# Optimization experiments

Measured on AMD Instinct MI355X. Metric: run time of the kernel, lower is better.

Reference implementation:

```python
import jax, jax.numpy as jnp
import numpy as np

B, T, H = 8, 2048, 1024
P = 64           # num_attention_project
N = 4096         # config.n (bias table length), N >= 2T-1
WINDOW = 64      # relative_attention
NEG = -10000.0


def setup_inputs() -> dict:
    key = jax.random.key(0)
    ks = jax.random.split(key, 10)
    s = 1.0 / np.sqrt(H)
    sp = 1.0 / np.sqrt(P)
    sb = 1.0 / np.sqrt(N)
    return {
        "attn_input": jax.random.normal(ks[0], (B, T, H), dtype=jnp.float32),
        "attention_mask": jnp.ones((B, T), dtype=jnp.float32),
        # Linear weights stored as [in, out] so y = x @ W + b
        "Wq": jax.random.uniform(ks[1], (H, P), minval=-s, maxval=s),
        "bq": jnp.zeros((P,), jnp.float32),
        "Wk": jax.random.uniform(ks[2], (H, P), minval=-s, maxval=s),
        "bk": jnp.zeros((P,), jnp.float32),
        "Wv": jax.random.uniform(ks[3], (H, P), minval=-s, maxval=s),
        "bv": jnp.zeros((P,), jnp.float32),
        "Wo": jax.random.uniform(ks[4], (P, H), minval=-sp, maxval=sp),
        "bo": jnp.zeros((H,), jnp.float32),
        "bias": jax.random.uniform(ks[5], (N,), minval=-sb, maxval=sb),
    }


def reference(attn_input, attention_mask, Wq, bq, Wk, bk, Wv, bv, Wo, bo, bias):
    q = attn_input @ Wq + bq            # [B,T,P]
    k = attn_input @ Wk + bk
    v = attn_input @ Wv + bv
    scores = jnp.einsum("btp,bsp->bts", q, k) / jnp.sqrt(jnp.float32(P))  # [B,T,T]
    # padding mask: note original broadcasts over COLUMNS via unsqueeze(-1)
    scores = scores + (1.0 - attention_mask)[:, :, None] * NEG
    # circulant window mask: keep |i-j| <= WINDOW (all ones if WINDOW >= T)
    i = jnp.arange(T)
    rel = i[:, None] - i[None, :]       # i - j
    win = (jnp.abs(rel) <= WINDOW) | (WINDOW >= T)
    scores = scores + jnp.where(win, 0.0, NEG)[None, :, :]
    # gathered learnable relative-position bias: bias[n//2 - i + j]
    scores = scores + bias[N // 2 - rel][None, :, :]
    attn = jax.nn.softmax(scores, axis=-1)
    out = jnp.einsum("bts,bsp->btp", attn, v)
    return out @ Wo + bo                # [B,T,H]
```

## Files before the change

### kernel.cpp

```cpp
#include <hip/hip_runtime.h>

using bf16x8 = __attribute__((ext_vector_type(8))) short;
using f32x4  = __attribute__((ext_vector_type(4))) float;

static __device__ inline unsigned short f2bf(float f) {
  unsigned int u = __float_as_uint(f);
  u += 0x7fffu + ((u >> 16) & 1u);
  return (unsigned short)(u >> 16);
}
static __device__ inline unsigned int pk2(float a, float b) {
  return (unsigned int)f2bf(a) | ((unsigned int)f2bf(b) << 16);
}

#define ROW16_MAX(x) { \
  { int _t = __builtin_amdgcn_update_dpp(0, __float_as_int(x), 0x121, 0xf, 0xf, true); x = fmaxf(x, __int_as_float(_t)); } \
  { int _t = __builtin_amdgcn_update_dpp(0, __float_as_int(x), 0x122, 0xf, 0xf, true); x = fmaxf(x, __int_as_float(_t)); } \
  { int _t = __builtin_amdgcn_update_dpp(0, __float_as_int(x), 0x124, 0xf, 0xf, true); x = fmaxf(x, __int_as_float(_t)); } \
  { int _t = __builtin_amdgcn_update_dpp(0, __float_as_int(x), 0x128, 0xf, 0xf, true); x = fmaxf(x, __int_as_float(_t)); } }
#define ROW16_SUM(x) { \
  { int _t = __builtin_amdgcn_update_dpp(0, __float_as_int(x), 0x121, 0xf, 0xf, true); x += __int_as_float(_t); } \
  { int _t = __builtin_amdgcn_update_dpp(0, __float_as_int(x), 0x122, 0xf, 0xf, true); x += __int_as_float(_t); } \
  { int _t = __builtin_amdgcn_update_dpp(0, __float_as_int(x), 0x124, 0xf, 0xf, true); x += __int_as_float(_t); } \
  { int _t = __builtin_amdgcn_update_dpp(0, __float_as_int(x), 0x128, 0xf, 0xf, true); x += __int_as_float(_t); } }

__global__ __launch_bounds__(256) void prep_kernel(
    const float* __restrict__ Wq, const float* __restrict__ Wk, const float* __restrict__ Wv,
    const float* __restrict__ Wo, const float* __restrict__ bq, const float* __restrict__ bk,
    const float* __restrict__ bv,
    unsigned short* __restrict__ Wt, unsigned short* __restrict__ Wot, float* __restrict__ bqkv)
{
  int idx = blockIdx.x * 256 + threadIdx.x;
  if (idx < 192 * 1024) {
    int n = idx >> 10, k = idx & 1023;
    const float* W = (n < 64) ? Wq : (n < 128) ? Wk : Wv;
    Wt[idx] = f2bf(W[k * 64 + (n & 63)]);
  } else if (idx < 192 * 1024 + 1024 * 64) {
    int j = idx - 192 * 1024;
    int n = j >> 6, k = j & 63;
    Wot[j] = f2bf(Wo[k * 1024 + n]);
  } else if (idx < 192 * 1024 + 1024 * 64 + 192) {
    int n = idx - (192 * 1024 + 1024 * 64);
    bqkv[n] = (n < 64) ? bq[n] : (n < 128) ? bk[n - 64] : bv[n - 128];
  }
}

__global__ __launch_bounds__(256) void qkv_gemm(
    const float* __restrict__ X, const unsigned short* __restrict__ Wt,
    const float* __restrict__ bqkv, unsigned short* __restrict__ qkvb)
{
  __shared__ __align__(16) unsigned short As[2][32 * 72];
  __shared__ __align__(16) unsigned short Bs[2][96 * 72];
  int t = threadIdx.x;
  int lane = t & 63, w = t >> 6;
  int m0 = (blockIdx.x >> 1) * 32;
  int nbase = (blockIdx.x & 1) * 96;
  int mg = w & 1, ng = w >> 1;
  int col = lane & 15, quad = lane >> 4;
  f32x4 acc[3] = {};

  int rowA = t >> 3, cA = t & 7;
  const float* srcA = X + (size_t)(m0 + rowA) * 1024 + cA * 8;
  const unsigned short* srcB = Wt + (size_t)(nbase + rowA) * 1024 + cA * 8;

  float4 f0 = *(const float4*)(srcA);
  float4 f1 = *(const float4*)(srcA + 4);
  uint4 b0 = *(const uint4*)(srcB);
  uint4 b1 = *(const uint4*)(srcB + 32 * 1024);
  uint4 b2 = *(const uint4*)(srcB + 64 * 1024);

  for (int ks = 0; ks < 16; ++ks) {
    int cur = ks & 1;
    {
      uint4 p;
      p.x = pk2(f0.x, f0.y); p.y = pk2(f0.z, f0.w);
      p.z = pk2(f1.x, f1.y); p.w = pk2(f1.z, f1.w);
      *(uint4*)(As[cur] + rowA * 72 + cA * 8) = p;
      *(uint4*)(Bs[cur] + rowA * 72 + cA * 8) = b0;
      *(uint4*)(Bs[cur] + (rowA + 32) * 72 + cA * 8) = b1;
      *(uint4*)(Bs[cur] + (rowA + 64) * 72 + cA * 8) = b2;
    }
    if (ks < 15) {
      const float* sA = srcA + (ks + 1) * 64;
      f0 = *(const float4*)(sA);
      f1 = *(const float4*)(sA + 4);
      const unsigned short* sB = srcB + (ks + 1) * 64;
      b0 = *(const uint4*)(sB);
      b1 = *(const uint4*)(sB + 32 * 1024);
      b2 = *(const uint4*)(sB + 64 * 1024);
    }
    __syncthreads();
    #pragma unroll
    for (int kk = 0; kk < 64; kk += 32) {
      int ko = kk + quad * 8;
      bf16x8 a = *(const bf16x8*)(As[cur] + (mg * 16 + col) * 72 + ko);
      #pragma unroll
      for (int ns = 0; ns < 3; ++ns) {
        bf16x8 b = *(const bf16x8*)(Bs[cur] + ((ng * 3 + ns) * 16 + col) * 72 + ko);
        acc[ns] = __builtin_amdgcn_mfma_f32_16x16x32_bf16(a, b, acc[ns], 0, 0, 0);
      }
    }
  }
  #pragma unroll
  for (int ns = 0; ns < 3; ++ns)
    #pragma unroll
    for (int r = 0; r < 4; ++r) {
      int m = m0 + mg * 16 + quad * 4 + r;
      int n = nbase + ng * 48 + ns * 16 + col;
      qkvb[(size_t)m * 192 + n] = f2bf(acc[ns][r] + bqkv[n]);
    }
}

__global__ __launch_bounds__(256) void band_attn(
    const unsigned short* __restrict__ qkvb, const float* __restrict__ bias,
    unsigned short* __restrict__ attnout)
{
  __shared__ __align__(16) unsigned short Kl[192 * 72];
  __shared__ __align__(16) unsigned short Vt[64 * 216];
  __shared__ __align__(16) unsigned short Ps[4 * 16 * 168];
  __shared__ float biasL[129];

  int t = threadIdx.x;
  int lane = t & 63, w = t >> 6;
  int col = lane & 15, quad = lane >> 4;
  int bidx = blockIdx.x;
  int b = bidx >> 5;
  int i0 = (bidx & 31) * 64;
  int jw = i0 - 64;
  const unsigned short* qbase = qkvb + (size_t)(b << 11) * 192;

  int iq = i0 + w * 16;
  const unsigned short* qr = qbase + (size_t)(iq + col) * 192 + quad * 8;
  bf16x8 aq0 = *(const bf16x8*)(qr);
  bf16x8 aq1 = *(const bf16x8*)(qr + 32);

  if (t < 129) biasL[t] = bias[1984 + t];
  #pragma unroll
  for (int it = 0; it < 12; ++it) {
    int idx = it * 256 + t;
    int row = idx >> 4;
    int c = idx & 15;
    int jb = jw + row;
    int jc = jb < 0 ? 0 : (jb > 2047 ? 2047 : jb);
    const unsigned short* src = qbase + (size_t)jc * 192 + 64 + c * 8;
    uint4 v = *(const uint4*)src;
    if (c < 8) {
      *(uint4*)(Kl + row * 72 + c * 8) = v;
    } else {
      union { uint4 u; unsigned short s[8]; } uv; uv.u = v;
      int p0 = (c - 8) * 8;
      #pragma unroll
      for (int e = 0; e < 8; ++e) Vt[(p0 + e) * 216 + row] = uv.s[e];
    }
  }
  {
    int p = t >> 2, c0 = 192 + (t & 3) * 4;
    *(uint2*)(Vt + p * 216 + c0) = make_uint2(0u, 0u);
  }
  __syncthreads();

  f32x4 s[9];
  #pragma unroll
  for (int t9 = 0; t9 < 9; ++t9) {
    int krow = ((w + t9) * 16 + col) * 72;
    bf16x8 kb0 = *(const bf16x8*)(Kl + krow + quad * 8);
    bf16x8 kb1 = *(const bf16x8*)(Kl + krow + 32 + quad * 8);
    f32x4 z = {};
    z = __builtin_amdgcn_mfma_f32_16x16x32_bf16(aq0, kb0, z, 0, 0, 0);
    s[t9] = __builtin_amdgcn_mfma_f32_16x16x32_bf16(aq1, kb1, z, 0, 0, 0);
  }
  int q4 = quad * 4;
  float mrow[4] = {-3e38f, -3e38f, -3e38f, -3e38f};
  #pragma unroll
  for (int t9 = 0; t9 < 9; ++t9) {
    int j = iq - 64 + t9 * 16 + col;
    #pragma unroll
    for (int r = 0; r < 4; ++r) {
      int diff = q4 + r + 64 - t9 * 16 - col;
      bool valid = (j >= 0) & (j < 2048) & (diff >= -64) & (diff <= 64);
      int bi = 64 - diff; bi = bi < 0 ? 0 : (bi > 128 ? 128 : bi);
      float sv = valid ? (s[t9][r] * 0.125f + biasL[bi]) : -3e38f;
      s[t9][r] = sv;
      mrow[r] = fmaxf(mrow[r], sv);
    }
  }
  #pragma unroll
  for (int r = 0; r < 4; ++r) ROW16_MAX(mrow[r]);
  unsigned short* Pw = Ps + w * (16 * 168);
  float lsum[4] = {0.f, 0.f, 0.f, 0.f};
  #pragma unroll
  for (int t9 = 0; t9 < 9; ++t9)
    #pragma unroll
    for (int r = 0; r < 4; ++r) {
      float p = __expf(s[t9][r] - mrow[r]);
      lsum[r] += p;
      Pw[(q4 + r) * 168 + t9 * 16 + col] = f2bf(p);
    }
  #pragma unroll
  for (int r = 0; r < 4; ++r) {
    ROW16_SUM(lsum[r]);
    Pw[(q4 + r) * 168 + 144 + col] = 0;
  }
  f32x4 o[4] = {};
  #pragma unroll
  for (int kc = 0; kc < 5; ++kc) {
    bf16x8 pa = *(const bf16x8*)(Pw + col * 168 + kc * 32 + quad * 8);
    #pragma unroll
    for (int nt = 0; nt < 4; ++nt) {
      bf16x8 vb = *(const bf16x8*)(Vt + (nt * 16 + col) * 216 + 16 * w + kc * 32 + quad * 8);
      o[nt] = __builtin_amdgcn_mfma_f32_16x16x32_bf16(pa, vb, o[nt], 0, 0, 0);
    }
  }
  float rl[4];
  #pragma unroll
  for (int r = 0; r < 4; ++r) rl[r] = 1.0f / lsum[r];
  #pragma unroll
  for (int nt = 0; nt < 4; ++nt)
    #pragma unroll
    for (int r = 0; r < 4; ++r) {
      int arow = (b << 11) + iq + q4 + r;
      attnout[(size_t)arow * 64 + nt * 16 + col] = f2bf(o[nt][r] * rl[r]);
    }
}

__global__ __launch_bounds__(256) void out_gemm(
    const unsigned short* __restrict__ attn, const unsigned short* __restrict__ Wot,
    const float* __restrict__ bo, float* __restrict__ out)
{
  __shared__ __align__(16) unsigned short As[64 * 72];
  __shared__ __align__(16) unsigned short Bs[128 * 72];
  int t = threadIdx.x, lane = t & 63, w = t >> 6;
  int m0 = (blockIdx.x >> 3) * 64;
  int n0 = (blockIdx.x & 7) * 128;
  #pragma unroll
  for (int r = 0; r < 2; ++r) {
    int tau = t + 256 * r; int row = tau >> 3, c = tau & 7;
    *(uint4*)(As + row * 72 + c * 8) =
        *(const uint4*)(attn + (size_t)(m0 + row) * 64 + c * 8);
  }
  #pragma unroll
  for (int r = 0; r < 4; ++r) {
    int tau = t + 256 * r; int n = tau >> 3, c = tau & 7;
    *(uint4*)(Bs + n * 72 + c * 8) =
        *(const uint4*)(Wot + (size_t)(n0 + n) * 64 + c * 8);
  }
  __syncthreads();
  f32x4 acc[2][4] = {};
  int mg = w & 1, ngg = w >> 1;
  #pragma unroll
  for (int kk = 0; kk < 64; kk += 32) {
    int ko = kk + (lane >> 4) * 8;
    bf16x8 a0 = *(const bf16x8*)(As + (mg * 32 +      (lane & 15)) * 72 + ko);
    bf16x8 a1 = *(const bf16x8*)(As + (mg * 32 + 16 + (lane & 15)) * 72 + ko);
    #pragma unroll
    for (int ns = 0; ns < 4; ++ns) {
      bf16x8 b = *(const bf16x8*)(Bs + ((ngg * 4 + ns) * 16 + (lane & 15)) * 72 + ko);
      acc[0][ns] = __builtin_amdgcn_mfma_f32_16x16x32_bf16(a0, b, acc[0][ns], 0, 0, 0);
      acc[1][ns] = __builtin_amdgcn_mfma_f32_16x16x32_bf16(a1, b, acc[1][ns], 0, 0, 0);
    }
  }
  int col = lane & 15, q = lane >> 4;
  #pragma unroll
  for (int ms = 0; ms < 2; ++ms)
    #pragma unroll
    for (int ns = 0; ns < 4; ++ns)
      #pragma unroll
      for (int r = 0; r < 4; ++r) {
        int mm = m0 + mg * 32 + ms * 16 + q * 4 + r;
        int nn = n0 + (ngg * 4 + ns) * 16 + col;
        out[(size_t)mm * 1024 + nn] = acc[ms][ns][r] + bo[nn];
      }
}

extern "C" void kernel_launch(void* const* d_in, const int* in_sizes, int n_in,
                              void* d_out, int out_size, void* d_ws, size_t ws_size,
                              hipStream_t stream) {
  const float* X    = (const float*)d_in[0];
  const float* Wq   = (const float*)d_in[2];
  const float* bq   = (const float*)d_in[3];
  const float* Wk   = (const float*)d_in[4];
  const float* bk   = (const float*)d_in[5];
  const float* Wv   = (const float*)d_in[6];
  const float* bv   = (const float*)d_in[7];
  const float* Wo   = (const float*)d_in[8];
  const float* bo   = (const float*)d_in[9];
  const float* bias = (const float*)d_in[10];
  float* out = (float*)d_out;
  char* ws = (char*)d_ws;
  unsigned short* qkvb = (unsigned short*)(ws);
  unsigned short* attn = (unsigned short*)(ws + 6291456);
  unsigned short* Wt   = (unsigned short*)(ws + 8388608);
  unsigned short* Wot  = (unsigned short*)(ws + 8781824);
  float*          bqkv = (float*)(ws + 8912896);

  prep_kernel<<<1025, 256, 0, stream>>>(Wq, Wk, Wv, Wo, bq, bk, bv, Wt, Wot, bqkv);
  qkv_gemm<<<1024, 256, 0, stream>>>(X, Wt, bqkv, qkvb);
  band_attn<<<256, 256, 0, stream>>>(qkvb, bias, attn);
  out_gemm<<<2048, 256, 0, stream>>>(attn, Wot, bo, out);
}
```

Before: 167.7 us.

## Split band attention key tiles across wave pairs and unroll QKV GEMM double buffer

The band attention kernel now runs with 512 threads. Each pair of waves splits the 9 key tiles and the 5 PV k-chunks of one 16-row query strip, and the pair combines row max, row sum and partial outputs through shared memory. This raises occupancy and parallelism for a kernel launched with only 256 blocks, at the cost of extra syncs and shared memory. The QKV GEMM loop is also manually unrolled by two with separate register sets for even and odd stages, which removes the dynamic buffer index.

Result: no change. 167.5 us (-0.1%).

```diff
diff --git a/kernel.cpp b/kernel.cpp
--- a/kernel.cpp
+++ b/kernel.cpp
@@ -44,6 +44,34 @@
   }
 }
 
+#define QKV_STORE(BUF, A0, A1, B0, B1, B2) { \
+  uint4 pv_; \
+  pv_.x = pk2(A0.x, A0.y); pv_.y = pk2(A0.z, A0.w); \
+  pv_.z = pk2(A1.x, A1.y); pv_.w = pk2(A1.z, A1.w); \
+  *(uint4*)(As[BUF] + rowA * 72 + cA * 8) = pv_; \
+  *(uint4*)(Bs[BUF] + rowA * 72 + cA * 8) = B0; \
+  *(uint4*)(Bs[BUF] + (rowA + 32) * 72 + cA * 8) = B1; \
+  *(uint4*)(Bs[BUF] + (rowA + 64) * 72 + cA * 8) = B2; }
+
+#define QKV_LOAD(KS, A0, A1, B0, B1, B2) { \
+  const float* sA_ = srcA + (KS) * 64; \
+  A0 = *(const float4*)(sA_); A1 = *(const float4*)(sA_ + 4); \
+  const unsigned short* sB_ = srcB + (KS) * 64; \
+  B0 = *(const uint4*)(sB_); \
+  B1 = *(const uint4*)(sB_ + 32 * 1024); \
+  B2 = *(const uint4*)(sB_ + 64 * 1024); }
+
+#define QKV_MMA(BUF) { \
+  _Pragma("unroll") \
+  for (int kk = 0; kk < 64; kk += 32) { \
+    int ko = kk + quad * 8; \
+    bf16x8 afr = *(const bf16x8*)(As[BUF] + (mg * 16 + col) * 72 + ko); \
+    _Pragma("unroll") \
+    for (int ns = 0; ns < 3; ++ns) { \
+      bf16x8 bfr = *(const bf16x8*)(Bs[BUF] + ((ng * 3 + ns) * 16 + col) * 72 + ko); \
+      acc[ns] = __builtin_amdgcn_mfma_f32_16x16x32_bf16(afr, bfr, acc[ns], 0, 0, 0); \
+    } } }
+
 __global__ __launch_bounds__(256) void qkv_gemm(
     const float* __restrict__ X, const unsigned short* __restrict__ Wt,
     const float* __restrict__ bqkv, unsigned short* __restrict__ qkvb)
@@ -62,43 +90,20 @@
   const float* srcA = X + (size_t)(m0 + rowA) * 1024 + cA * 8;
   const unsigned short* srcB = Wt + (size_t)(nbase + rowA) * 1024 + cA * 8;
 
-  float4 f0 = *(const float4*)(srcA);
-  float4 f1 = *(const float4*)(srcA + 4);
-  uint4 b0 = *(const uint4*)(srcB);
-  uint4 b1 = *(const uint4*)(srcB + 32 * 1024);
-  uint4 b2 = *(const uint4*)(srcB + 64 * 1024);
-
-  for (int ks = 0; ks < 16; ++ks) {
-    int cur = ks & 1;
-    {
-      uint4 p;
-      p.x = pk2(f0.x, f0.y); p.y = pk2(f0.z, f0.w);
-      p.z = pk2(f1.x, f1.y); p.w = pk2(f1.z, f1.w);
-      *(uint4*)(As[cur] + rowA * 72 + cA * 8) = p;
-      *(uint4*)(Bs[cur] + rowA * 72 + cA * 8) = b0;
-      *(uint4*)(Bs[cur] + (rowA + 32) * 72 + cA * 8) = b1;
-      *(uint4*)(Bs[cur] + (rowA + 64) * 72 + cA * 8) = b2;
-    }
-    if (ks < 15) {
-      const float* sA = srcA + (ks + 1) * 64;
-      f0 = *(const float4*)(sA);
-      f1 = *(const float4*)(sA + 4);
-      const unsigned short* sB = srcB + (ks + 1) * 64;
-      b0 = *(const uint4*)(sB);
-      b1 = *(const uint4*)(sB + 32 * 1024);
-      b2 = *(const uint4*)(sB + 64 * 1024);
-    }
+  float4 eA0, eA1; uint4 eB0, eB1, eB2;
+  float4 oA0, oA1; uint4 oB0, oB1, oB2;
+  QKV_LOAD(0, eA0, eA1, eB0, eB1, eB2);
+  QKV_LOAD(1, oA0, oA1, oB0, oB1, oB2);
+
+  for (int ks = 0; ks < 16; ks += 2) {
+    QKV_STORE(0, eA0, eA1, eB0, eB1, eB2);
+    if (ks + 2 < 16) QKV_LOAD(ks + 2, eA0, eA1, eB0, eB1, eB2);
     __syncthreads();
-    #pragma unroll
-    for (int kk = 0; kk < 64; kk += 32) {
-      int ko = kk + quad * 8;
-      bf16x8 a = *(const bf16x8*)(As[cur] + (mg * 16 + col) * 72 + ko);
-      #pragma unroll
-      for (int ns = 0; ns < 3; ++ns) {
-        bf16x8 b = *(const bf16x8*)(Bs[cur] + ((ng * 3 + ns) * 16 + col) * 72 + ko);
-        acc[ns] = __builtin_amdgcn_mfma_f32_16x16x32_bf16(a, b, acc[ns], 0, 0, 0);
-      }
-    }
+    QKV_MMA(0);
+    QKV_STORE(1, oA0, oA1, oB0, oB1, oB2);
+    if (ks + 3 < 16) QKV_LOAD(ks + 3, oA0, oA1, oB0, oB1, oB2);
+    __syncthreads();
+    QKV_MMA(1);
   }
   #pragma unroll
   for (int ns = 0; ns < 3; ++ns)
@@ -110,33 +115,37 @@
     }
 }
 
-__global__ __launch_bounds__(256) void band_attn(
+__global__ __launch_bounds__(512) void band_attn(
     const unsigned short* __restrict__ qkvb, const float* __restrict__ bias,
     unsigned short* __restrict__ attnout)
 {
   __shared__ __align__(16) unsigned short Kl[192 * 72];
   __shared__ __align__(16) unsigned short Vt[64 * 216];
   __shared__ __align__(16) unsigned short Ps[4 * 16 * 168];
+  __shared__ float Osum[4][16][64];
+  __shared__ float Mx[8][16];
+  __shared__ float Lx[8][16];
   __shared__ float biasL[129];
 
   int t = threadIdx.x;
   int lane = t & 63, w = t >> 6;
-  int col = lane & 15, quad = lane >> 4;
+  int p = w >> 1, s = w & 1;
+  int col = lane & 15, quad = lane >> 4, q4 = quad * 4;
   int bidx = blockIdx.x;
   int b = bidx >> 5;
   int i0 = (bidx & 31) * 64;
   int jw = i0 - 64;
   const unsigned short* qbase = qkvb + (size_t)(b << 11) * 192;
 
-  int iq = i0 + w * 16;
+  int iq = i0 + p * 16;
   const unsigned short* qr = qbase + (size_t)(iq + col) * 192 + quad * 8;
   bf16x8 aq0 = *(const bf16x8*)(qr);
   bf16x8 aq1 = *(const bf16x8*)(qr + 32);
 
   if (t < 129) biasL[t] = bias[1984 + t];
   #pragma unroll
-  for (int it = 0; it < 12; ++it) {
-    int idx = it * 256 + t;
+  for (int it = 0; it < 6; ++it) {
+    int idx = it * 512 + t;
     int row = idx >> 4;
     int c = idx & 15;
     int jb = jw + row;
@@ -146,80 +155,110 @@
     if (c < 8) {
       *(uint4*)(Kl + row * 72 + c * 8) = v;
     } else {
-      union { uint4 u; unsigned short s[8]; } uv; uv.u = v;
+      union { uint4 u; unsigned short ss[8]; } uv; uv.u = v;
       int p0 = (c - 8) * 8;
       #pragma unroll
-      for (int e = 0; e < 8; ++e) Vt[(p0 + e) * 216 + row] = uv.s[e];
-    }
-  }
-  {
-    int p = t >> 2, c0 = 192 + (t & 3) * 4;
-    *(uint2*)(Vt + p * 216 + c0) = make_uint2(0u, 0u);
-  }
-  __syncthreads();
-
-  f32x4 s[9];
-  #pragma unroll
-  for (int t9 = 0; t9 < 9; ++t9) {
-    int krow = ((w + t9) * 16 + col) * 72;
+      for (int e = 0; e < 8; ++e) Vt[(p0 + e) * 216 + row] = uv.ss[e];
+    }
+  }
+  if (t < 256) {
+    int pz = t >> 2, c0 = 192 + (t & 3) * 4;
+    *(uint2*)(Vt + pz * 216 + c0) = make_uint2(0u, 0u);
+  }
+  __syncthreads();
+
+  int nt9 = 5 - s, t9b = 5 * s;
+  f32x4 sv[5];
+  for (int i = 0; i < nt9; ++i) {
+    int t9 = t9b + i;
+    int krow = ((p + t9) * 16 + col) * 72;
     bf16x8 kb0 = *(const bf16x8*)(Kl + krow + quad * 8);
     bf16x8 kb1 = *(const bf16x8*)(Kl + krow + 32 + quad * 8);
     f32x4 z = {};
     z = __builtin_amdgcn_mfma_f32_16x16x32_bf16(aq0, kb0, z, 0, 0, 0);
-    s[t9] = __builtin_amdgcn_mfma_f32_16x16x32_bf16(aq1, kb1, z, 0, 0, 0);
-  }
-  int q4 = quad * 4;
+    sv[i] = __builtin_amdgcn_mfma_f32_16x16x32_bf16(aq1, kb1, z, 0, 0, 0);
+  }
   float mrow[4] = {-3e38f, -3e38f, -3e38f, -3e38f};
-  #pragma unroll
-  for (int t9 = 0; t9 < 9; ++t9) {
+  for (int i = 0; i < nt9; ++i) {
+    int t9 = t9b + i;
     int j = iq - 64 + t9 * 16 + col;
     #pragma unroll
     for (int r = 0; r < 4; ++r) {
       int diff = q4 + r + 64 - t9 * 16 - col;
       bool valid = (j >= 0) & (j < 2048) & (diff >= -64) & (diff <= 64);
       int bi = 64 - diff; bi = bi < 0 ? 0 : (bi > 128 ? 128 : bi);
-      float sv = valid ? (s[t9][r] * 0.125f + biasL[bi]) : -3e38f;
-      s[t9][r] = sv;
-      mrow[r] = fmaxf(mrow[r], sv);
+      float x = valid ? (sv[i][r] * 0.125f + biasL[bi]) : -3e38f;
+      sv[i][r] = x;
+      mrow[r] = fmaxf(mrow[r], x);
     }
   }
   #pragma unroll
   for (int r = 0; r < 4; ++r) ROW16_MAX(mrow[r]);
-  unsigned short* Pw = Ps + w * (16 * 168);
+  if (col == 0) {
+    #pragma unroll
+    for (int r = 0; r < 4; ++r) Mx[w][q4 + r] = mrow[r];
+  }
+  __syncthreads();
+  #pragma unroll
+  for (int r = 0; r < 4; ++r) mrow[r] = fmaxf(mrow[r], Mx[w ^ 1][q4 + r]);
+
+  unsigned short* Pw = Ps + p * (16 * 168);
   float lsum[4] = {0.f, 0.f, 0.f, 0.f};
-  #pragma unroll
-  for (int t9 = 0; t9 < 9; ++t9)
+  for (int i = 0; i < nt9; ++i) {
+    int t9 = t9b + i;
     #pragma unroll
     for (int r = 0; r < 4; ++r) {
-      float p = __expf(s[t9][r] - mrow[r]);
-      lsum[r] += p;
-      Pw[(q4 + r) * 168 + t9 * 16 + col] = f2bf(p);
-    }
-  #pragma unroll
-  for (int r = 0; r < 4; ++r) {
-    ROW16_SUM(lsum[r]);
-    Pw[(q4 + r) * 168 + 144 + col] = 0;
-  }
+      float pe = __expf(sv[i][r] - mrow[r]);
+      lsum[r] += pe;
+      Pw[(q4 + r) * 168 + t9 * 16 + col] = f2bf(pe);
+    }
+  }
+  #pragma unroll
+  for (int r = 0; r < 4; ++r) ROW16_SUM(lsum[r]);
+  if (col == 0) {
+    #pragma unroll
+    for (int r = 0; r < 4; ++r) Lx[w][q4 + r] = lsum[r];
+  }
+  if (s == 0) {
+    #pragma unroll
+    for (int r = 0; r < 4; ++r) Pw[(q4 + r) * 168 + 144 + col] = 0;
+  }
+  __syncthreads();
+  #pragma unroll
+  for (int r = 0; r < 4; ++r) lsum[r] += Lx[w ^ 1][q4 + r];
+
   f32x4 o[4] = {};
-  #pragma unroll
-  for (int kc = 0; kc < 5; ++kc) {
+  int nkc = 3 - s, kcb = 3 * s;
+  for (int i = 0; i < nkc; ++i) {
+    int kc = kcb + i;
     bf16x8 pa = *(const bf16x8*)(Pw + col * 168 + kc * 32 + quad * 8);
     #pragma unroll
     for (int nt = 0; nt < 4; ++nt) {
-      bf16x8 vb = *(const bf16x8*)(Vt + (nt * 16 + col) * 216 + 16 * w + kc * 32 + quad * 8);
+      bf16x8 vb = *(const bf16x8*)(Vt + (nt * 16 + col) * 216 + 16 * p + kc * 32 + quad * 8);
       o[nt] = __builtin_amdgcn_mfma_f32_16x16x32_bf16(pa, vb, o[nt], 0, 0, 0);
     }
   }
-  float rl[4];
-  #pragma unroll
-  for (int r = 0; r < 4; ++r) rl[r] = 1.0f / lsum[r];
-  #pragma unroll
-  for (int nt = 0; nt < 4; ++nt)
-    #pragma unroll
-    for (int r = 0; r < 4; ++r) {
-      int arow = (b << 11) + iq + q4 + r;
-      attnout[(size_t)arow * 64 + nt * 16 + col] = f2bf(o[nt][r] * rl[r]);
-    }
+  if (s == 1) {
+    #pragma unroll
+    for (int nt = 0; nt < 4; ++nt)
+      #pragma unroll
+      for (int r = 0; r < 4; ++r)
+        Osum[p][q4 + r][nt * 16 + col] = o[nt][r];
+  }
+  __syncthreads();
+  if (s == 0) {
+    float rl[4];
+    #pragma unroll
+    for (int r = 0; r < 4; ++r) rl[r] = 1.0f / lsum[r];
+    #pragma unroll
+    for (int nt = 0; nt < 4; ++nt)
+      #pragma unroll
+      for (int r = 0; r < 4; ++r) {
+        int arow = (b << 11) + iq + q4 + r;
+        attnout[(size_t)arow * 64 + nt * 16 + col] =
+            f2bf((o[nt][r] + Osum[p][q4 + r][nt * 16 + col]) * rl[r]);
+      }
+  }
 }
 
 __global__ __launch_bounds__(256) void out_gemm(
@@ -294,6 +333,6 @@
 
   prep_kernel<<<1025, 256, 0, stream>>>(Wq, Wk, Wv, Wo, bq, bk, bv, Wt, Wot, bqkv);
   qkv_gemm<<<1024, 256, 0, stream>>>(X, Wt, bqkv, qkvb);
-  band_attn<<<256, 256, 0, stream>>>(qkvb, bias, attn);
+  band_attn<<<256, 512, 0, stream>>>(qkvb, bias, attn);
   out_gemm<<<2048, 256, 0, stream>>>(attn, Wot, bo, out);
 }
```
